# Kernel tuning notes

Hardware: AMD Instinct MI355X
Metric: run time of the kernel (lower is better)

Reference implementation:

```python
import jax, jax.numpy as jnp
import numpy as np

B, S, D = 2, 2048, 2048
H, KV, HD = 8, 2, 256
EPS = 1e-6
WINDOW = 512
ROPE_THETA = 1000000.0
NEG = -1e9


def setup_inputs() -> dict:
    key = jax.random.key(0)
    ks = jax.random.split(key, 6)
    hidden_states = jax.random.normal(ks[0], (B, S, D), dtype=jnp.float32)
    # rotary tables: [S, HD//2] freqs tiled to [B, S, HD]
    inv_freq = 1.0 / (ROPE_THETA ** (np.arange(0, HD, 2, dtype=np.float32) / HD))
    pos = np.arange(S, dtype=np.float32)
    freqs = np.outer(pos, inv_freq)                      # [S, HD/2]
    emb = np.concatenate([freqs, freqs], axis=-1)        # [S, HD]
    cos = jnp.broadcast_to(jnp.asarray(np.cos(emb))[None], (B, S, HD))
    sin = jnp.broadcast_to(jnp.asarray(np.sin(emb))[None], (B, S, HD))
    # causal sliding-window additive mask: allow k<=q and q-k < WINDOW
    q_idx = np.arange(S)[:, None]
    k_idx = np.arange(S)[None, :]
    allowed = (k_idx <= q_idx) & (q_idx - k_idx < WINDOW)
    attention_mask = jnp.asarray(np.where(allowed, 0.0, NEG).astype(np.float32))[None, None]
    sc = 0.02
    wq = jax.random.normal(ks[1], (D, H * HD), dtype=jnp.float32) * sc
    wk = jax.random.normal(ks[2], (D, KV * HD), dtype=jnp.float32) * sc
    wv = jax.random.normal(ks[3], (D, KV * HD), dtype=jnp.float32) * sc
    wo = jax.random.normal(ks[4], (H * HD, D), dtype=jnp.float32) * sc
    q_norm_w = jnp.ones((HD,), dtype=jnp.float32)
    k_norm_w = jnp.ones((HD,), dtype=jnp.float32)
    return dict(hidden_states=hidden_states, cos=cos, sin=sin,
                attention_mask=attention_mask, wq=wq, wk=wk, wv=wv, wo=wo,
                q_norm_w=q_norm_w, k_norm_w=k_norm_w)


def _rms_norm(x, w):
    xf = x.astype(jnp.float32)
    y = xf * jax.lax.rsqrt(jnp.mean(xf * xf, axis=-1, keepdims=True) + EPS)
    return (y * w).astype(x.dtype)


def _apply_rope(x, cos, sin):
    # x: [B, S, N, HD]; cos/sin: [B, S, HD] -> unsqueeze at dim 2
    c = cos[:, :, None, :]
    s = sin[:, :, None, :]
    x1, x2 = jnp.split(x, 2, axis=-1)
    rot = jnp.concatenate([-x2, x1], axis=-1)
    return x * c + rot * s


def reference(hidden_states, cos, sin, attention_mask, wq, wk, wv, wo,
              q_norm_w, k_norm_w):
    b, s, _ = hidden_states.shape
    n_rep = H // KV
    q = (hidden_states @ wq).reshape(b, s, H, HD)
    q = _apply_rope(_rms_norm(q, q_norm_w), cos, sin).transpose(0, 2, 1, 3)   # [B,H,S,HD]
    k = (hidden_states @ wk).reshape(b, s, KV, HD)
    k = _apply_rope(_rms_norm(k, k_norm_w), cos, sin).transpose(0, 2, 1, 3)   # [B,KV,S,HD]
    v = (hidden_states @ wv).reshape(b, s, KV, HD)
    v = _rms_norm(v, jnp.float32(1.0)).transpose(0, 2, 1, 3)                  # [B,KV,S,HD]
    k = jnp.repeat(k, n_rep, axis=1)  # GQA repeat_kv -> [B,H,S,HD]
    v = jnp.repeat(v, n_rep, axis=1)
    # Gemma3n uses scaling = 1.0 (QK-RMSNorm replaces 1/sqrt(d))
    scores = jnp.einsum('bhqd,bhkd->bhqk', q, k) + attention_mask[:, :, :, :s]
    probs = jax.nn.softmax(scores.astype(jnp.float32), axis=-1).astype(q.dtype)
    out = jnp.einsum('bhqk,bhkd->bhqd', probs, v)
    out = out.transpose(0, 2, 1, 3).reshape(b, s, H * HD)
    return out @ wo
```

## Files before the change

### kernel.cpp

```cpp
#include <hip/hip_runtime.h>
#include <hip/hip_bf16.h>
#include <hip/hip_fp16.h>

#define B_ 2
#define S_ 2048
#define D_ 2048
#define H_ 8
#define KV_ 2
#define HD_ 256
#define WINDOW_ 512
#define EPS_ 1e-6f
#define MASKV_ -30000.0f

typedef _Float16 f16;
typedef _Float16 half8 __attribute__((ext_vector_type(8)));
typedef _Float16 half2v __attribute__((ext_vector_type(2)));
typedef _Float16 half4v __attribute__((ext_vector_type(4)));
typedef float floatx4 __attribute__((ext_vector_type(4)));

#define GLOAD_LDS16(g, l)                                                        \
    __builtin_amdgcn_global_load_lds(                                            \
        (const __attribute__((address_space(1))) unsigned int*)(g),              \
        (__attribute__((address_space(3))) unsigned int*)(l), 16, 0, 0)

__global__ __launch_bounds__(256) void prep(const float* __restrict__ x,
                                            const float* __restrict__ wq,
                                            const float* __restrict__ wk,
                                            const float* __restrict__ wv,
                                            const float* __restrict__ wo,
                                            f16* __restrict__ xh,
                                            f16* __restrict__ BT,
                                            f16* __restrict__ woT) {
    int bid = blockIdx.x;
    const int t = threadIdx.x;
    if (bid < 8192) {
        const int i = bid * 256 + t;
        float4 v = ((const float4*)x)[i];
        half4v hv = {(f16)v.x, (f16)v.y, (f16)v.z, (f16)v.w};
        ((half4v*)xh)[i] = hv;
        return;
    }
    bid -= 8192;
    const float* src;
    f16* dst;
    int C, bx, by;
    if (bid < 4096) {
        src = wq; dst = BT; C = 2048; bx = bid & 63; by = bid >> 6;
    } else if (bid < 5120) {
        const int b2 = bid - 4096;
        src = wk; dst = BT + (size_t)2048 * 2048; C = 512; bx = b2 & 15; by = b2 >> 4;
    } else if (bid < 6144) {
        const int b2 = bid - 5120;
        src = wv; dst = BT + (size_t)2560 * 2048; C = 512; bx = b2 & 15; by = b2 >> 4;
    } else {
        const int b2 = bid - 6144;
        src = wo; dst = woT; C = 2048; bx = b2 & 63; by = b2 >> 6;
    }
    __shared__ float tile[32][33];
    const int tx = t & 31, ty = t >> 5;
    const int c0 = bx * 32, r0 = by * 32;
#pragma unroll
    for (int i = 0; i < 4; ++i)
        tile[ty + i * 8][tx] = src[(size_t)(r0 + ty + i * 8) * C + c0 + tx];
    __syncthreads();
#pragma unroll
    for (int i = 0; i < 4; ++i)
        dst[(size_t)(c0 + ty + i * 8) * 2048 + r0 + tx] = (f16)tile[tx][ty + i * 8];
}

template <typename OutT>
__global__ __launch_bounds__(256) void gemm_f16(const f16* __restrict__ A,
                                                const f16* __restrict__ BT,
                                                OutT* __restrict__ C,
                                                int M, int N, int K) {
    __shared__ __align__(16) f16 sA[128 * 32];
    __shared__ __align__(16) f16 sB[128 * 32];

    const int t = threadIdx.x;
    const int lane = t & 63;
    const int w = t >> 6;
    const int i16 = lane & 15, q4 = lane >> 4;
    const int m0 = blockIdx.y * 128, n0 = blockIdx.x * 128;
    const int mw = (w & 1) * 64, nw = (w >> 1) * 64;

    floatx4 acc[16];
#pragma unroll
    for (int i = 0; i < 16; ++i) acc[i] = (floatx4){0.f, 0.f, 0.f, 0.f};

    const int srow = w * 32 + (lane >> 2);
    const int sgp = lane & 3;

    for (int k0 = 0; k0 < K; k0 += 32) {
#pragma unroll
        for (int c = 0; c < 2; ++c) {
            const int chunk = w * 2 + c;
            const int row = srow + c * 16;
            const int g = (sgp - (row >> 1)) & 3;
            GLOAD_LDS16(A + (size_t)(m0 + row) * K + k0 + g * 8,
                        sA + chunk * 512 + lane * 8);
            GLOAD_LDS16(BT + (size_t)(n0 + row) * K + k0 + g * 8,
                        sB + chunk * 512 + lane * 8);
        }
        __syncthreads();

        half8 af[4], bf[4];
#pragma unroll
        for (int mi = 0; mi < 4; ++mi) {
            const int row = mw + mi * 16 + i16;
            const int gp = (q4 + (row >> 1)) & 3;
            af[mi] = *(const half8*)(sA + row * 32 + gp * 8);
        }
#pragma unroll
        for (int ni = 0; ni < 4; ++ni) {
            const int row = nw + ni * 16 + i16;
            const int gp = (q4 + (row >> 1)) & 3;
            bf[ni] = *(const half8*)(sB + row * 32 + gp * 8);
        }
#pragma unroll
        for (int mi = 0; mi < 4; ++mi)
#pragma unroll
            for (int ni = 0; ni < 4; ++ni)
                acc[mi * 4 + ni] = __builtin_amdgcn_mfma_f32_16x16x32_f16(
                    af[mi], bf[ni], acc[mi * 4 + ni], 0, 0, 0);
        __syncthreads();
    }

#pragma unroll
    for (int mi = 0; mi < 4; ++mi)
#pragma unroll
        for (int ni = 0; ni < 4; ++ni)
#pragma unroll
            for (int r = 0; r < 4; ++r) {
                const int row = m0 + mw + mi * 16 + q4 * 4 + r;
                const int col = n0 + nw + ni * 16 + i16;
                C[(size_t)row * N + col] = (OutT)acc[mi * 4 + ni][r];
            }
}

#define NRB_ ((B_ * S_ * (H_ + KV_)) / 4)

__global__ __launch_bounds__(256) void norm_rope_f16(
    f16* __restrict__ QKVh, f16* __restrict__ Kh, f16* __restrict__ Vt,
    const float* __restrict__ cosb, const float* __restrict__ sinb,
    const float* __restrict__ qw, const float* __restrict__ kw) {
    __shared__ f16 vt[64][266];

    const int w = threadIdx.x >> 6, lane = threadIdx.x & 63;

    if (blockIdx.x < NRB_) {
        const int wid = blockIdx.x * 4 + w;
        const int nq = B_ * S_ * H_;
        const int d0 = lane * 2;

        if (wid < nq) {
            const int b = wid / (S_ * H_);
            const int r = wid % (S_ * H_);
            const int s = r / H_, h = r % H_;
            f16* p = QKVh + (size_t)(b * S_ + s) * 3072 + h * HD_;
            half2v lo = *(const half2v*)(p + d0);
            half2v hi = *(const half2v*)(p + 128 + d0);
            float x0 = (float)lo[0], x1 = (float)lo[1], x2 = (float)hi[0], x3 = (float)hi[1];
            float ss = x0 * x0 + x1 * x1 + x2 * x2 + x3 * x3;
#pragma unroll
            for (int off = 32; off >= 1; off >>= 1) ss += __shfl_xor(ss, off);
            const float inv = rsqrtf(ss * (1.0f / HD_) + EPS_);
            float2 wlo = *(const float2*)(qw + d0), whi = *(const float2*)(qw + 128 + d0);
            float y0 = x0 * inv * wlo.x, y1 = x1 * inv * wlo.y;
            float y2 = x2 * inv * whi.x, y3 = x3 * inv * whi.y;
            const float* cb = cosb + (size_t)(b * S_ + s) * HD_;
            const float* sb = sinb + (size_t)(b * S_ + s) * HD_;
            float2 clo = *(const float2*)(cb + d0), chi = *(const float2*)(cb + 128 + d0);
            float2 slo = *(const float2*)(sb + d0), shi = *(const float2*)(sb + 128 + d0);
            half2v olo = {(f16)(y0 * clo.x - y2 * slo.x), (f16)(y1 * clo.y - y3 * slo.y)};
            half2v ohi = {(f16)(y2 * chi.x + y0 * shi.x), (f16)(y3 * chi.y + y1 * shi.y)};
            *(half2v*)(p + d0) = olo;
            *(half2v*)(p + 128 + d0) = ohi;
        } else {
            const int idx = wid - nq;
            const int b = idx / (S_ * KV_);
            const int r = idx % (S_ * KV_);
            const int s = r / KV_, kv = r % KV_;
            const f16* p = QKVh + (size_t)(b * S_ + s) * 3072 + 2048 + kv * HD_;
            half2v lo = *(const half2v*)(p + d0);
            half2v hi = *(const half2v*)(p + 128 + d0);
            float x0 = (float)lo[0], x1 = (float)lo[1], x2 = (float)hi[0], x3 = (float)hi[1];
            float ss = x0 * x0 + x1 * x1 + x2 * x2 + x3 * x3;
#pragma unroll
            for (int off = 32; off >= 1; off >>= 1) ss += __shfl_xor(ss, off);
            const float inv = rsqrtf(ss * (1.0f / HD_) + EPS_);
            float2 wlo = *(const float2*)(kw + d0), whi = *(const float2*)(kw + 128 + d0);
            float y0 = x0 * inv * wlo.x, y1 = x1 * inv * wlo.y;
            float y2 = x2 * inv * whi.x, y3 = x3 * inv * whi.y;
            const float* cb = cosb + (size_t)(b * S_ + s) * HD_;
            const float* sb = sinb + (size_t)(b * S_ + s) * HD_;
            float2 clo = *(const float2*)(cb + d0), chi = *(const float2*)(cb + 128 + d0);
            float2 slo = *(const float2*)(sb + d0), shi = *(const float2*)(sb + 128 + d0);
            half2v olo = {(f16)(y0 * clo.x - y2 * slo.x), (f16)(y1 * clo.y - y3 * slo.y)};
            half2v ohi = {(f16)(y2 * chi.x + y0 * shi.x), (f16)(y3 * chi.y + y1 * shi.y)};
            f16* d = Kh + ((size_t)(b * KV_ + kv) * S_ + s) * HD_;
            *(half2v*)(d + d0) = olo;
            *(half2v*)(d + 128 + d0) = ohi;
        }
        return;
    }

    const int vb = blockIdx.x - NRB_;
    const int s0 = (vb & 31) * 64;
    const int kv = (vb >> 5) & 1;
    const int b  = vb >> 6;

    for (int r = 0; r < 16; ++r) {
        const int sl = w * 16 + r;
        const f16* p = QKVh + (size_t)(b * S_ + s0 + sl) * 3072 + 2560 + kv * HD_;
        const int d0 = lane * 2;
        half2v lo = *(const half2v*)(p + d0);
        half2v hi = *(const half2v*)(p + 128 + d0);
        float x0 = (float)lo[0], x1 = (float)lo[1], x2 = (float)hi[0], x3 = (float)hi[1];
        float ss = x0 * x0 + x1 * x1 + x2 * x2 + x3 * x3;
#pragma unroll
        for (int off = 32; off >= 1; off >>= 1) ss += __shfl_xor(ss, off);
        const float inv = rsqrtf(ss * (1.0f / HD_) + EPS_);
        half2v olo = {(f16)(x0 * inv), (f16)(x1 * inv)};
        half2v ohi = {(f16)(x2 * inv), (f16)(x3 * inv)};
        *(half2v*)&vt[sl][d0] = olo;
        *(half2v*)&vt[sl][128 + d0] = ohi;
    }
    __syncthreads();
    f16* dst = Vt + (size_t)(b * KV_ + kv) * HD_ * S_;
    for (int i = 0; i < 64; ++i) {
        const int dd = w * 64 + i;
        dst[(size_t)dd * S_ + s0 + lane] = vt[lane][dd];
    }
}

__global__ __launch_bounds__(512, 2) void attn_mfma(const f16* __restrict__ QKVh,
                                                    const f16* __restrict__ Kh,
                                                    const f16* __restrict__ Vt,
                                                    f16* __restrict__ attnh) {
    __shared__ __align__(16) f16 sK[2][64 * 256];
    __shared__ __align__(16) f16 sV[2][256 * 64];
    __shared__ __align__(16) f16 sP[8][16 * 72];

    const int qt = blockIdx.x, h = blockIdx.y, b = blockIdx.z;
    const int kvh = h / (H_ / KV_);
    const int t = threadIdx.x, lane = t & 63, w = t >> 6;
    const int i16 = lane & 15, q4 = lane >> 4;

    const int qrow = qt * 128 + w * 16 + i16;
    const f16* qbase = QKVh + (size_t)(b * S_ + qrow) * 3072 + h * HD_ + q4 * 8;
    half8 qf[8];
#pragma unroll
    for (int kk = 0; kk < 8; ++kk) qf[kk] = *(const half8*)(qbase + kk * 32);

    floatx4 o[16];
#pragma unroll
    for (int i = 0; i < 16; ++i) o[i] = (floatx4){0.f, 0.f, 0.f, 0.f};
    float mrow[4] = {-1e30f, -1e30f, -1e30f, -1e30f};
    float lrow[4] = {0.f, 0.f, 0.f, 0.f};

    const size_t kbase = (size_t)(b * KV_ + kvh) * S_ * HD_;
    const size_t vbase = (size_t)(b * KV_ + kvh) * HD_ * S_;
    const int srow0 = qt * 128 + w * 16 + q4 * 4;

    const int kt_lo = (2 * qt - 8) > 0 ? (2 * qt - 8) : 0;
    const int kt_hi = 2 * qt + 1;
    const int s_lo_w = qt * 128 + w * 16;
    int ktw_lo = (s_lo_w - (WINDOW_ - 1)) >> 6;
    if (ktw_lo < kt_lo) ktw_lo = kt_lo;
    const int ktw_hi = (s_lo_w + 15) >> 6;

    auto stage = [&](int kt, int buf) {
#pragma unroll
        for (int c = 0; c < 4; ++c) {
            const int chunk = w * 4 + c;
            const int keyl = chunk * 2 + (lane >> 5);
            const int g = (lane & 31) ^ (keyl & 31);
            GLOAD_LDS16(Kh + kbase + (size_t)(kt * 64 + keyl) * HD_ + g * 8,
                        sK[buf] + chunk * 512 + lane * 8);
            const int diml = chunk * 8 + (lane >> 3);
            const int g2 = (lane & 7) ^ (diml & 7);
            GLOAD_LDS16(Vt + vbase + (size_t)diml * S_ + kt * 64 + g2 * 8,
                        sV[buf] + chunk * 512 + lane * 8);
        }
    };

    stage(kt_lo, 0);
    int cur = 0;
    for (int kt = kt_lo; kt <= kt_hi; ++kt, cur ^= 1) {
        __syncthreads();
        if (kt < kt_hi) stage(kt + 1, cur ^ 1);
        if (kt < ktw_lo || kt > ktw_hi) continue;

        const f16* sKc = sK[cur];
        const f16* sVc = sV[cur];

        floatx4 sc[4];
#pragma unroll
        for (int nt = 0; nt < 4; ++nt) sc[nt] = (floatx4){0.f, 0.f, 0.f, 0.f};
#pragma unroll
        for (int ks = 0; ks < 8; ++ks)
#pragma unroll
            for (int nt = 0; nt < 4; ++nt) {
                const int keyl = nt * 16 + i16;
                const int gp = (ks * 4 + q4) ^ (keyl & 31);
                half8 kf = *(const half8*)(sKc + keyl * 256 + gp * 8);
                sc[nt] = __builtin_amdgcn_mfma_f32_16x16x32_f16(qf[ks], kf, sc[nt], 0, 0, 0);
            }

#pragma unroll
        for (int r = 0; r < 4; ++r) {
            const int s = srow0 + r;
            float mx = -1e30f;
#pragma unroll
            for (int nt = 0; nt < 4; ++nt) {
                const int j = kt * 64 + nt * 16 + i16;
                const bool valid = (j <= s) && (s - j < WINDOW_);
                const float v = valid ? sc[nt][r] : MASKV_;
                sc[nt][r] = v;
                mx = fmaxf(mx, v);
            }
#pragma unroll
            for (int off = 1; off < 16; off <<= 1) mx = fmaxf(mx, __shfl_xor(mx, off));
            const float mnew = fmaxf(mrow[r], mx);
            const float alpha = __expf(mrow[r] - mnew);
            mrow[r] = mnew;
            float rs = 0.f;
#pragma unroll
            for (int nt = 0; nt < 4; ++nt) {
                const float p = __expf(sc[nt][r] - mnew);
                sc[nt][r] = p;
                rs += p;
            }
#pragma unroll
            for (int off = 1; off < 16; off <<= 1) rs += __shfl_xor(rs, off);
            lrow[r] = lrow[r] * alpha + rs;
#pragma unroll
            for (int nt2 = 0; nt2 < 16; ++nt2) o[nt2][r] *= alpha;
        }

        f16* sPw = sP[w];
#pragma unroll
        for (int nt = 0; nt < 4; ++nt)
#pragma unroll
            for (int r = 0; r < 4; ++r)
                sPw[(q4 * 4 + r) * 72 + nt * 16 + i16] = (f16)sc[nt][r];
        asm volatile("s_waitcnt lgkmcnt(0)" ::: "memory");

#pragma unroll
        for (int kt2 = 0; kt2 < 2; ++kt2) {
            half8 pf = *(const half8*)(sPw + i16 * 72 + kt2 * 32 + q4 * 8);
#pragma unroll
            for (int nt2 = 0; nt2 < 16; ++nt2) {
                const int dim = nt2 * 16 + i16;
                const int gp = (kt2 * 4 + q4) ^ (dim & 7);
                half8 vf = *(const half8*)(sVc + dim * 64 + gp * 8);
                o[nt2] = __builtin_amdgcn_mfma_f32_16x16x32_f16(pf, vf, o[nt2], 0, 0, 0);
            }
        }
    }

    float inv[4];
#pragma unroll
    for (int r = 0; r < 4; ++r) inv[r] = 1.0f / lrow[r];
    f16* ob = attnh + (size_t)(b * S_ + qt * 128 + w * 16) * (H_ * HD_) + h * HD_;
#pragma unroll
    for (int nt2 = 0; nt2 < 16; ++nt2)
#pragma unroll
        for (int r = 0; r < 4; ++r)
            ob[(size_t)(q4 * 4 + r) * (H_ * HD_) + nt2 * 16 + i16] =
                (f16)(o[nt2][r] * inv[r]);
}

extern "C" void kernel_launch(void* const* d_in, const int* in_sizes, int n_in,
                              void* d_out, int out_size, void* d_ws, size_t ws_size,
                              hipStream_t stream) {
    const float* x    = (const float*)d_in[0];
    const float* cosb = (const float*)d_in[1];
    const float* sinb = (const float*)d_in[2];
    const float* wq = (const float*)d_in[4];
    const float* wk = (const float*)d_in[5];
    const float* wv = (const float*)d_in[6];
    const float* wo = (const float*)d_in[7];
    const float* qw = (const float*)d_in[8];
    const float* kw = (const float*)d_in[9];
    float* out = (float*)d_out;

    f16* ws = (f16*)d_ws;
    f16* xh    = ws;
    f16* BT    = xh + 8388608;
    f16* woT   = BT + 6291456;
    f16* QKVh  = woT + 4194304;
    f16* Kh    = QKVh + 12582912;
    f16* Vt    = Kh + 2097152;
    f16* attnh = xh;

    const int M = B_ * S_;

    prep<<<18432, 256, 0, stream>>>(x, wq, wk, wv, wo, xh, BT, woT);

    gemm_f16<f16><<<dim3(24, 32), 256, 0, stream>>>(xh, BT, QKVh, M, 3072, D_);

    norm_rope_f16<<<NRB_ + 128, 256, 0, stream>>>(QKVh, Kh, Vt, cosb, sinb, qw, kw);

    attn_mfma<<<dim3(S_ / 128, H_, B_), 512, 0, stream>>>(QKVh, Kh, Vt, attnh);

    gemm_f16<float><<<dim3(16, 32), 256, 0, stream>>>(attnh, woT, out, M, D_, H_ * HD_);
}
```

Before: 339.1 us.

## Fuse Q norm/RoPE into attention, widen GEMM K-tile, vectorize weight transpose

Q RMSNorm and RoPE now run inside the attention kernel on the Q fragments held in registers, so the separate pass that read and rewrote Q in global memory is gone and the norm kernel handles only K and V. The GEMM K-step grows from 32 to 64 with an XOR-swizzled LDS layout, which halves the number of barriers per K and doubles shared-memory use per block. The weight-transpose prep kernel uses 64x64 tiles with float4 loads and half4 stores, cutting the block count. The trade-off is extra register pressure and cos/sin/weight loads inside attention.

```diff
diff --git a/kernel.cpp b/kernel.cpp
--- a/kernel.cpp
+++ b/kernel.cpp
@@ -17,6 +17,7 @@
 typedef _Float16 half2v __attribute__((ext_vector_type(2)));
 typedef _Float16 half4v __attribute__((ext_vector_type(4)));
 typedef float floatx4 __attribute__((ext_vector_type(4)));
+typedef float floatx8 __attribute__((ext_vector_type(8)));
 
 #define GLOAD_LDS16(g, l)                                                        \
     __builtin_amdgcn_global_load_lds(                                            \
@@ -44,28 +45,39 @@
     const float* src;
     f16* dst;
     int C, bx, by;
-    if (bid < 4096) {
-        src = wq; dst = BT; C = 2048; bx = bid & 63; by = bid >> 6;
-    } else if (bid < 5120) {
-        const int b2 = bid - 4096;
-        src = wk; dst = BT + (size_t)2048 * 2048; C = 512; bx = b2 & 15; by = b2 >> 4;
-    } else if (bid < 6144) {
-        const int b2 = bid - 5120;
-        src = wv; dst = BT + (size_t)2560 * 2048; C = 512; bx = b2 & 15; by = b2 >> 4;
+    if (bid < 1024) {
+        src = wq; dst = BT; C = 2048; bx = bid & 31; by = bid >> 5;
+    } else if (bid < 1280) {
+        const int b3 = bid - 1024;
+        src = wk; dst = BT + (size_t)2048 * 2048; C = 512; bx = b3 & 7; by = b3 >> 3;
+    } else if (bid < 1536) {
+        const int b3 = bid - 1280;
+        src = wv; dst = BT + (size_t)2560 * 2048; C = 512; bx = b3 & 7; by = b3 >> 3;
     } else {
-        const int b2 = bid - 6144;
-        src = wo; dst = woT; C = 2048; bx = b2 & 63; by = b2 >> 6;
-    }
-    __shared__ float tile[32][33];
-    const int tx = t & 31, ty = t >> 5;
-    const int c0 = bx * 32, r0 = by * 32;
-#pragma unroll
-    for (int i = 0; i < 4; ++i)
-        tile[ty + i * 8][tx] = src[(size_t)(r0 + ty + i * 8) * C + c0 + tx];
+        const int b3 = bid - 1536;
+        src = wo; dst = woT; C = 2048; bx = b3 & 31; by = b3 >> 5;
+    }
+    __shared__ float tl[64][65];
+    const int c0 = bx * 64, r0 = by * 64;
+#pragma unroll
+    for (int i = 0; i < 4; ++i) {
+        const int idx = i * 256 + t;
+        const int row = idx >> 4;
+        const int c4 = (idx & 15) * 4;
+        float4 v = *(const float4*)&src[(size_t)(r0 + row) * C + c0 + c4];
+        tl[row][c4 + 0] = v.x; tl[row][c4 + 1] = v.y;
+        tl[row][c4 + 2] = v.z; tl[row][c4 + 3] = v.w;
+    }
     __syncthreads();
 #pragma unroll
-    for (int i = 0; i < 4; ++i)
-        dst[(size_t)(c0 + ty + i * 8) * 2048 + r0 + tx] = (f16)tile[tx][ty + i * 8];
+    for (int i = 0; i < 4; ++i) {
+        const int idx = i * 256 + t;
+        const int c = idx >> 4;
+        const int r4 = (idx & 15) * 4;
+        half4v hv = {(f16)tl[r4 + 0][c], (f16)tl[r4 + 1][c],
+                     (f16)tl[r4 + 2][c], (f16)tl[r4 + 3][c]};
+        *(half4v*)&dst[(size_t)(c0 + c) * 2048 + r0 + r4] = hv;
+    }
 }
 
 template <typename OutT>
@@ -73,8 +85,8 @@
                                                 const f16* __restrict__ BT,
                                                 OutT* __restrict__ C,
                                                 int M, int N, int K) {
-    __shared__ __align__(16) f16 sA[128 * 32];
-    __shared__ __align__(16) f16 sB[128 * 32];
+    __shared__ __align__(16) f16 sA[128 * 64];
+    __shared__ __align__(16) f16 sB[128 * 64];
 
     const int t = threadIdx.x;
     const int lane = t & 63;
@@ -87,15 +99,14 @@
 #pragma unroll
     for (int i = 0; i < 16; ++i) acc[i] = (floatx4){0.f, 0.f, 0.f, 0.f};
 
-    const int srow = w * 32 + (lane >> 2);
-    const int sgp = lane & 3;
-
-    for (int k0 = 0; k0 < K; k0 += 32) {
-#pragma unroll
-        for (int c = 0; c < 2; ++c) {
-            const int chunk = w * 2 + c;
-            const int row = srow + c * 16;
-            const int g = (sgp - (row >> 1)) & 3;
+    const int r8 = lane >> 3;
+    const int g = (lane & 7) ^ r8;
+
+    for (int k0 = 0; k0 < K; k0 += 64) {
+#pragma unroll
+        for (int cc = 0; cc < 4; ++cc) {
+            const int chunk = w * 4 + cc;
+            const int row = chunk * 8 + r8;
             GLOAD_LDS16(A + (size_t)(m0 + row) * K + k0 + g * 8,
                         sA + chunk * 512 + lane * 8);
             GLOAD_LDS16(BT + (size_t)(n0 + row) * K + k0 + g * 8,
@@ -103,25 +114,27 @@
         }
         __syncthreads();
 
-        half8 af[4], bf[4];
-#pragma unroll
-        for (int mi = 0; mi < 4; ++mi) {
-            const int row = mw + mi * 16 + i16;
-            const int gp = (q4 + (row >> 1)) & 3;
-            af[mi] = *(const half8*)(sA + row * 32 + gp * 8);
-        }
-#pragma unroll
-        for (int ni = 0; ni < 4; ++ni) {
-            const int row = nw + ni * 16 + i16;
-            const int gp = (q4 + (row >> 1)) & 3;
-            bf[ni] = *(const half8*)(sB + row * 32 + gp * 8);
-        }
+        half8 af[2][4], bf[2][4];
+#pragma unroll
+        for (int kb = 0; kb < 2; ++kb)
+#pragma unroll
+            for (int mi = 0; mi < 4; ++mi) {
+                const int ra = mw + mi * 16 + i16;
+                const int ga = (kb * 4 + q4) ^ (ra & 7);
+                af[kb][mi] = *(const half8*)(sA + (ra >> 3) * 512 + (ra & 7) * 64 + ga * 8);
+                const int rb = nw + mi * 16 + i16;
+                const int gb = (kb * 4 + q4) ^ (rb & 7);
+                bf[kb][mi] = *(const half8*)(sB + (rb >> 3) * 512 + (rb & 7) * 64 + gb * 8);
+            }
 #pragma unroll
         for (int mi = 0; mi < 4; ++mi)
 #pragma unroll
-            for (int ni = 0; ni < 4; ++ni)
+            for (int ni = 0; ni < 4; ++ni) {
                 acc[mi * 4 + ni] = __builtin_amdgcn_mfma_f32_16x16x32_f16(
-                    af[mi], bf[ni], acc[mi * 4 + ni], 0, 0, 0);
+                    af[0][mi], bf[0][ni], acc[mi * 4 + ni], 0, 0, 0);
+                acc[mi * 4 + ni] = __builtin_amdgcn_mfma_f32_16x16x32_f16(
+                    af[1][mi], bf[1][ni], acc[mi * 4 + ni], 0, 0, 0);
+            }
         __syncthreads();
     }
 
@@ -137,74 +150,46 @@
             }
 }
 
-#define NRB_ ((B_ * S_ * (H_ + KV_)) / 4)
-
-__global__ __launch_bounds__(256) void norm_rope_f16(
-    f16* __restrict__ QKVh, f16* __restrict__ Kh, f16* __restrict__ Vt,
+#define NRBK_ ((B_ * S_ * KV_) / 4)
+
+__global__ __launch_bounds__(256) void norm_kv_f16(
+    const f16* __restrict__ QKVh, f16* __restrict__ Kh, f16* __restrict__ Vt,
     const float* __restrict__ cosb, const float* __restrict__ sinb,
-    const float* __restrict__ qw, const float* __restrict__ kw) {
+    const float* __restrict__ kw) {
     __shared__ f16 vt[64][266];
 
     const int w = threadIdx.x >> 6, lane = threadIdx.x & 63;
 
-    if (blockIdx.x < NRB_) {
+    if (blockIdx.x < NRBK_) {
         const int wid = blockIdx.x * 4 + w;
-        const int nq = B_ * S_ * H_;
         const int d0 = lane * 2;
-
-        if (wid < nq) {
-            const int b = wid / (S_ * H_);
-            const int r = wid % (S_ * H_);
-            const int s = r / H_, h = r % H_;
-            f16* p = QKVh + (size_t)(b * S_ + s) * 3072 + h * HD_;
-            half2v lo = *(const half2v*)(p + d0);
-            half2v hi = *(const half2v*)(p + 128 + d0);
-            float x0 = (float)lo[0], x1 = (float)lo[1], x2 = (float)hi[0], x3 = (float)hi[1];
-            float ss = x0 * x0 + x1 * x1 + x2 * x2 + x3 * x3;
-#pragma unroll
-            for (int off = 32; off >= 1; off >>= 1) ss += __shfl_xor(ss, off);
-            const float inv = rsqrtf(ss * (1.0f / HD_) + EPS_);
-            float2 wlo = *(const float2*)(qw + d0), whi = *(const float2*)(qw + 128 + d0);
-            float y0 = x0 * inv * wlo.x, y1 = x1 * inv * wlo.y;
-            float y2 = x2 * inv * whi.x, y3 = x3 * inv * whi.y;
-            const float* cb = cosb + (size_t)(b * S_ + s) * HD_;
-            const float* sb = sinb + (size_t)(b * S_ + s) * HD_;
-            float2 clo = *(const float2*)(cb + d0), chi = *(const float2*)(cb + 128 + d0);
-            float2 slo = *(const float2*)(sb + d0), shi = *(const float2*)(sb + 128 + d0);
-            half2v olo = {(f16)(y0 * clo.x - y2 * slo.x), (f16)(y1 * clo.y - y3 * slo.y)};
-            half2v ohi = {(f16)(y2 * chi.x + y0 * shi.x), (f16)(y3 * chi.y + y1 * shi.y)};
-            *(half2v*)(p + d0) = olo;
-            *(half2v*)(p + 128 + d0) = ohi;
-        } else {
-            const int idx = wid - nq;
-            const int b = idx / (S_ * KV_);
-            const int r = idx % (S_ * KV_);
-            const int s = r / KV_, kv = r % KV_;
-            const f16* p = QKVh + (size_t)(b * S_ + s) * 3072 + 2048 + kv * HD_;
-            half2v lo = *(const half2v*)(p + d0);
-            half2v hi = *(const half2v*)(p + 128 + d0);
-            float x0 = (float)lo[0], x1 = (float)lo[1], x2 = (float)hi[0], x3 = (float)hi[1];
-            float ss = x0 * x0 + x1 * x1 + x2 * x2 + x3 * x3;
-#pragma unroll
-            for (int off = 32; off >= 1; off >>= 1) ss += __shfl_xor(ss, off);
-            const float inv = rsqrtf(ss * (1.0f / HD_) + EPS_);
-            float2 wlo = *(const float2*)(kw + d0), whi = *(const float2*)(kw + 128 + d0);
-            float y0 = x0 * inv * wlo.x, y1 = x1 * inv * wlo.y;
-            float y2 = x2 * inv * whi.x, y3 = x3 * inv * whi.y;
-            const float* cb = cosb + (size_t)(b * S_ + s) * HD_;
-            const float* sb = sinb + (size_t)(b * S_ + s) * HD_;
-            float2 clo = *(const float2*)(cb + d0), chi = *(const float2*)(cb + 128 + d0);
-            float2 slo = *(const float2*)(sb + d0), shi = *(const float2*)(sb + 128 + d0);
-            half2v olo = {(f16)(y0 * clo.x - y2 * slo.x), (f16)(y1 * clo.y - y3 * slo.y)};
-            half2v ohi = {(f16)(y2 * chi.x + y0 * shi.x), (f16)(y3 * chi.y + y1 * shi.y)};
-            f16* d = Kh + ((size_t)(b * KV_ + kv) * S_ + s) * HD_;
-            *(half2v*)(d + d0) = olo;
-            *(half2v*)(d + 128 + d0) = ohi;
-        }
+        const int b = wid / (S_ * KV_);
+        const int r = wid % (S_ * KV_);
+        const int s = r / KV_, kv = r % KV_;
+        const f16* p = QKVh + (size_t)(b * S_ + s) * 3072 + 2048 + kv * HD_;
+        half2v lo = *(const half2v*)(p + d0);
+        half2v hi = *(const half2v*)(p + 128 + d0);
+        float x0 = (float)lo[0], x1 = (float)lo[1], x2 = (float)hi[0], x3 = (float)hi[1];
+        float ss = x0 * x0 + x1 * x1 + x2 * x2 + x3 * x3;
+#pragma unroll
+        for (int off = 32; off >= 1; off >>= 1) ss += __shfl_xor(ss, off);
+        const float inv = rsqrtf(ss * (1.0f / HD_) + EPS_);
+        float2 wlo = *(const float2*)(kw + d0), whi = *(const float2*)(kw + 128 + d0);
+        float y0 = x0 * inv * wlo.x, y1 = x1 * inv * wlo.y;
+        float y2 = x2 * inv * whi.x, y3 = x3 * inv * whi.y;
+        const float* cb = cosb + (size_t)(b * S_ + s) * HD_;
+        const float* sb = sinb + (size_t)(b * S_ + s) * HD_;
+        float2 clo = *(const float2*)(cb + d0), chi = *(const float2*)(cb + 128 + d0);
+        float2 slo = *(const float2*)(sb + d0), shi = *(const float2*)(sb + 128 + d0);
+        half2v olo = {(f16)(y0 * clo.x - y2 * slo.x), (f16)(y1 * clo.y - y3 * slo.y)};
+        half2v ohi = {(f16)(y2 * chi.x + y0 * shi.x), (f16)(y3 * chi.y + y1 * shi.y)};
+        f16* d = Kh + ((size_t)(b * KV_ + kv) * S_ + s) * HD_;
+        *(half2v*)(d + d0) = olo;
+        *(half2v*)(d + 128 + d0) = ohi;
         return;
     }
 
-    const int vb = blockIdx.x - NRB_;
+    const int vb = blockIdx.x - NRBK_;
     const int s0 = (vb & 31) * 64;
     const int kv = (vb >> 5) & 1;
     const int b  = vb >> 6;
@@ -236,7 +221,10 @@
 __global__ __launch_bounds__(512, 2) void attn_mfma(const f16* __restrict__ QKVh,
                                                     const f16* __restrict__ Kh,
                                                     const f16* __restrict__ Vt,
-                                                    f16* __restrict__ attnh) {
+                                                    f16* __restrict__ attnh,
+                                                    const float* __restrict__ cosb,
+                                                    const float* __restrict__ sinb,
+                                                    const float* __restrict__ qw) {
     __shared__ __align__(16) f16 sK[2][64 * 256];
     __shared__ __align__(16) f16 sV[2][256 * 64];
     __shared__ __align__(16) f16 sP[8][16 * 72];
@@ -251,6 +239,43 @@
     half8 qf[8];
 #pragma unroll
     for (int kk = 0; kk < 8; ++kk) qf[kk] = *(const half8*)(qbase + kk * 32);
+
+    {
+        float ss = 0.f;
+#pragma unroll
+        for (int kk = 0; kk < 8; ++kk)
+#pragma unroll
+            for (int j = 0; j < 8; ++j) {
+                const float v = (float)qf[kk][j];
+                ss += v * v;
+            }
+        ss += __shfl_xor(ss, 16);
+        ss += __shfl_xor(ss, 32);
+        const float inv = rsqrtf(ss * (1.0f / HD_) + EPS_);
+        const float* cb = cosb + (size_t)(b * S_ + qrow) * HD_ + q4 * 8;
+        const float* sb = sinb + (size_t)(b * S_ + qrow) * HD_ + q4 * 8;
+        const float* wp = qw + q4 * 8;
+#pragma unroll
+        for (int kk = 0; kk < 4; ++kk) {
+            const int dl = kk * 32, dh = dl + 128;
+            floatx8 cl = *(const floatx8*)(cb + dl);
+            floatx8 ch = *(const floatx8*)(cb + dh);
+            floatx8 sl = *(const floatx8*)(sb + dl);
+            floatx8 sh = *(const floatx8*)(sb + dh);
+            floatx8 wl = *(const floatx8*)(wp + dl);
+            floatx8 wh = *(const floatx8*)(wp + dh);
+            half8 nl, nh;
+#pragma unroll
+            for (int j = 0; j < 8; ++j) {
+                const float xl = (float)qf[kk][j] * inv * wl[j];
+                const float xh = (float)qf[kk + 4][j] * inv * wh[j];
+                nl[j] = (f16)(xl * cl[j] - xh * sl[j]);
+                nh[j] = (f16)(xh * ch[j] + xl * sh[j]);
+            }
+            qf[kk] = nl;
+            qf[kk + 4] = nh;
+        }
+    }
 
     floatx4 o[16];
 #pragma unroll
@@ -359,16 +384,16 @@
         }
     }
 
-    float inv[4];
-#pragma unroll
-    for (int r = 0; r < 4; ++r) inv[r] = 1.0f / lrow[r];
+    float inv2[4];
+#pragma unroll
+    for (int r = 0; r < 4; ++r) inv2[r] = 1.0f / lrow[r];
     f16* ob = attnh + (size_t)(b * S_ + qt * 128 + w * 16) * (H_ * HD_) + h * HD_;
 #pragma unroll
     for (int nt2 = 0; nt2 < 16; ++nt2)
 #pragma unroll
         for (int r = 0; r < 4; ++r)
             ob[(size_t)(q4 * 4 + r) * (H_ * HD_) + nt2 * 16 + i16] =
-                (f16)(o[nt2][r] * inv[r]);
+                (f16)(o[nt2][r] * inv2[r]);
 }
 
 extern "C" void kernel_launch(void* const* d_in, const int* in_sizes, int n_in,
@@ -396,13 +421,14 @@
 
     const int M = B_ * S_;
 
-    prep<<<18432, 256, 0, stream>>>(x, wq, wk, wv, wo, xh, BT, woT);
+    prep<<<8192 + 2560, 256, 0, stream>>>(x, wq, wk, wv, wo, xh, BT, woT);
 
     gemm_f16<f16><<<dim3(24, 32), 256, 0, stream>>>(xh, BT, QKVh, M, 3072, D_);
 
-    norm_rope_f16<<<NRB_ + 128, 256, 0, stream>>>(QKVh, Kh, Vt, cosb, sinb, qw, kw);
-
-    attn_mfma<<<dim3(S_ / 128, H_, B_), 512, 0, stream>>>(QKVh, Kh, Vt, attnh);
+    norm_kv_f16<<<NRBK_ + 128, 256, 0, stream>>>(QKVh, Kh, Vt, cosb, sinb, kw);
+
+    attn_mfma<<<dim3(S_ / 128, H_, B_), 512, 0, stream>>>(QKVh, Kh, Vt, attnh,
+                                                          cosb, sinb, qw);
 
     gemm_f16<float><<<dim3(16, 32), 256, 0, stream>>>(attnh, woT, out, M, D_, H_ * HD_);
 }
```

Result: faster. 325.2 us (-4.1%).
